# Kernel tuning notes

Measured on AMD Instinct MI355X. Metric: run time of the kernel, lower is better.

Reference implementation:

```python
import jax, jax.numpy as jnp
import numpy as np

B, IN, H, OUT, RANK = 2048, 256, 128, 128, 8
EPS = 1e-5

def setup_inputs() -> dict:
    key = jax.random.key(0)
    ks = jax.random.split(key, 9)
    inv = lambda n: 1.0 / np.sqrt(n)
    return {
        "X": jax.random.normal(ks[0], (B, IN), jnp.float32),
        "W1": jax.random.uniform(ks[1], (IN, H), jnp.float32, -inv(IN), inv(IN)),
        "b1": jnp.zeros((H,), jnp.float32),
        "W2": jax.random.uniform(ks[2], (IN, OUT), jnp.float32, -inv(IN), inv(IN)),
        "b2": jnp.zeros((OUT,), jnp.float32),
        "W3": jax.random.uniform(ks[3], (H, OUT), jnp.float32, -inv(H), inv(H)),
        "b3": jnp.zeros((OUT,), jnp.float32),
        "P": jax.random.normal(ks[4], (RANK, H, H, H), jnp.float32),  # (rank, p, q, k)
        "gz": jnp.ones((H,), jnp.float32),
        "bz": jnp.zeros((H,), jnp.float32),
        "gy": jnp.ones((H,), jnp.float32),
        "by": jnp.zeros((H,), jnp.float32),
    }

def _bn(x, g, b):
    # training-mode BatchNorm1d: batch stats, biased variance
    m = x.mean(axis=0)
    v = x.var(axis=0)
    return (x - m) * jax.lax.rsqrt(v + EPS) * g + b

def reference(X, W1, b1, W2, b2, W3, b3, P, gz, bz, gy, by):
    Z = jax.nn.relu(X @ W1 + b1)               # (B, H); dropout = identity (eval)

    def step(carry, Pi):
        Zi, Y = carry
        # batch_quadratic: out[b,k] = sum_{p,q} Zi[b,p] * Pi[p,q,k] * Z[b,q]
        Zi = jnp.einsum('bp,pqk,bq->bk', Zi, Pi, Z)
        Zi = _bn(Zi, gz, bz)
        return (Zi, Y + Zi / RANK), None

    Y0 = jnp.zeros((X.shape[0], H), X.dtype)
    (_, Y), _ = jax.lax.scan(step, (Z, Y0), P)
    Y = _bn(Y, gy, by)
    out = jax.nn.relu(jax.nn.relu(Y @ W3 + b3) + jax.nn.relu(X @ W2 + b2))
    return out
```

## Files before the change

### kernel.cpp

```cpp
#include <hip/hip_runtime.h>

typedef __bf16 bf16x8 __attribute__((ext_vector_type(8)));
typedef float  floatx4 __attribute__((ext_vector_type(4)));

constexpr int B_    = 2048;
constexpr int NIN   = 256;
constexpr int H_    = 128;
constexpr int RANK_ = 8;
constexpr float EPS_ = 1e-5f;

__global__ __launch_bounds__(256)
void k_head(const float* __restrict__ X,
            const float* __restrict__ W1, const float* __restrict__ b1,
            const float* __restrict__ W2, const float* __restrict__ b2,
            const float* __restrict__ P,
            float* __restrict__ Z, float* __restrict__ R2, __bf16* __restrict__ Zbf,
            __bf16* __restrict__ Pperm, float* __restrict__ stats ) {
    __shared__ float smem[10240];
    const int bx = blockIdx.x, t = threadIdx.x;

    if (bx < RANK_ + 1) stats[bx * 256 + t] = 0.f;

    if ((bx & 3) == 0) {
        const int b0 = (bx >> 2) * 8;
        float* sX  = smem;
        float* sW1 = smem + 2048;
        float* sW2 = smem + 6144;
        for (int e = t; e < 2048; e += 256) {
            const int row = e >> 8, i = e & 255;
            sX[e] = X[(size_t)(b0 + row) * NIN + i];
        }
        const int col = t & 127, rh = t >> 7;
        float s1[4] = {0.f, 0.f, 0.f, 0.f}, s2[4] = {0.f, 0.f, 0.f, 0.f};
        for (int c = 0; c < 8; ++c) {
            __syncthreads();
#pragma unroll
            for (int q = 0; q < 4; ++q) {
                const int idx = q * 256 + t;
                const int i = idx >> 5, c4 = idx & 31;
                *(float4*)&sW1[i * 128 + c4 * 4] =
                    *(const float4*)&W1[(size_t)(c * 32 + i) * H_ + c4 * 4];
                *(float4*)&sW2[i * 128 + c4 * 4] =
                    *(const float4*)&W2[(size_t)(c * 32 + i) * H_ + c4 * 4];
            }
            __syncthreads();
#pragma unroll 4
            for (int i = 0; i < 32; ++i) {
                const float w1 = sW1[i * 128 + col];
                const float w2 = sW2[i * 128 + col];
#pragma unroll
                for (int j = 0; j < 4; ++j) {
                    const float x = sX[(rh * 4 + j) * 256 + c * 32 + i];
                    s1[j] = fmaf(x, w1, s1[j]);
                    s2[j] = fmaf(x, w2, s2[j]);
                }
            }
        }
#pragma unroll
        for (int j = 0; j < 4; ++j) {
            const int b = b0 + rh * 4 + j;
            const float z = fmaxf(s1[j] + b1[col], 0.f);
            const float r = fmaxf(s2[j] + b2[col], 0.f);
            Z[(size_t)b * H_ + col]   = z;
            Zbf[(size_t)b * H_ + col] = (__bf16)z;
            R2[(size_t)b * H_ + col]  = r;
        }
        __syncthreads();
    }
    {
        float* sT = smem;
        const int r = bx >> 7, p = bx & 127;
        const float4* Pp4 = (const float4*)(P + ((size_t)r * H_ + p) * (H_ * H_));
        __bf16* dst = Pperm + (size_t)r * (H_ * H_ * H_);
        const int L = t & 63, quad = L >> 4, lo = L & 15, g0 = t >> 6;
#pragma unroll
        for (int s = 0; s < 4; ++s) {
#pragma unroll
            for (int it = 0; it < 4; ++it) {
                const int idx = it * 256 + t;
                const int q = idx >> 5, k4 = idx & 31;
                const float4 v = Pp4[(size_t)(s * 32 + q) * 32 + k4];
                float* d = sT + q * 129 + k4 * 4;
                d[0] = v.x; d[1] = v.y; d[2] = v.z; d[3] = v.w;
            }
            __syncthreads();
#pragma unroll
            for (int gg = 0; gg < 2; ++gg) {
                const int g = g0 + 4 * gg;
                __bf16 v8[8];
#pragma unroll
                for (int j = 0; j < 8; ++j)
                    v8[j] = (__bf16)sT[(quad * 8 + j) * 129 + g * 16 + lo];
                *(bf16x8*)(dst + (((size_t)(g * 128 + p) * 4 + s) * 64 + L) * 8) =
                    *(const bf16x8*)v8;
            }
            __syncthreads();
        }
    }
}

__global__ __launch_bounds__(1024, 1)
void k_rank(const __bf16* __restrict__ Pr, const __bf16* __restrict__ Zbf,
            const float* __restrict__ prevT, const float* __restrict__ prevStats,
            const float* __restrict__ gz, const float* __restrict__ bz,
            float* __restrict__ T, float* __restrict__ stats,
            float* __restrict__ Y, const int ymode) {
    __shared__ float smem[16672];
    const int kg = blockIdx.x, mblk = blockIdx.y, b0 = mblk * 64;
    const int t = threadIdx.x;
    const int w = t >> 6, L = t & 63, quad = L >> 4, lo = L & 15;

    float* sAl = smem + 16384; float* sBe = smem + 16512;
    if (t < 128) {
        if (ymode == 0) { sAl[t] = 1.f; sBe[t] = 0.f; }
        else {
            const float s1 = prevStats[t], s2 = prevStats[128 + t];
            const float mm = s1 * (1.f / B_);
            const float var = s2 * (1.f / B_) - mm * mm;
            const float a = rsqrtf(var + EPS_) * gz[t];
            sAl[t] = a; sBe[t] = bz[t] - mm * a;
        }
    }
    bf16x8 A[4][4];
#pragma unroll
    for (int mt = 0; mt < 4; ++mt)
#pragma unroll
        for (int ks = 0; ks < 4; ++ks)
            A[mt][ks] = *(const bf16x8*)(Zbf + (size_t)(b0 + mt * 16 + lo) * H_ + ks * 32 + quad * 8);
    __syncthreads();
    {
        const int sp = t & 127, rr = t >> 7;
        const float a = sAl[sp], be = sBe[sp];
#pragma unroll
        for (int i = 0; i < 8; ++i) {
            const int row = rr + 8 * i;
            const float zin = fmaf(prevT[(size_t)(b0 + row) * H_ + sp], a, be);
            smem[sp * 68 + row] = zin;
            if (kg == 0 && ymode != 0) {
                float* yp = Y + (size_t)(b0 + row) * H_ + sp;
                *yp = (ymode == 1) ? zin * (1.f / RANK_) : fmaf(zin, 1.f / RANK_, *yp);
            }
        }
    }
    __syncthreads();

    floatx4 acc[4];
#pragma unroll
    for (int mt = 0; mt < 4; ++mt) acc[mt] = (floatx4){0.f, 0.f, 0.f, 0.f};

    const bf16x8* Pb = (const bf16x8*)Pr;
    const size_t wb = ((size_t)kg * 128 + w * 8) * 4;
    for (int pp = 0; pp < 8; ++pp) {
        bf16x8 Bf[4];
#pragma unroll
        for (int s = 0; s < 4; ++s)
            Bf[s] = Pb[(wb + (size_t)pp * 4 + s) * 64 + L];
        const int p = w * 8 + pp;
#pragma unroll
        for (int mt = 0; mt < 4; ++mt) {
            floatx4 S = (floatx4){0.f, 0.f, 0.f, 0.f};
#pragma unroll
            for (int ks = 0; ks < 4; ++ks)
                S = __builtin_amdgcn_mfma_f32_16x16x32_bf16(A[mt][ks], Bf[ks], S, 0, 0, 0);
            const floatx4 zi = *(const floatx4*)&smem[p * 68 + mt * 16 + quad * 4];
            acc[mt] += zi * S;
        }
    }
    __syncthreads();
#pragma unroll
    for (int mt = 0; mt < 4; ++mt)
#pragma unroll
        for (int i = 0; i < 4; ++i)
            smem[w * 1024 + (mt * 4 + i) * 64 + L] = acc[mt][i];
    if (t < 32) smem[16640 + t] = 0.f;
    __syncthreads();

    float v = 0.f;
#pragma unroll
    for (int q = 0; q < 16; ++q) v += smem[q * 1024 + t];
    const int j = t >> 6, L2 = t & 63;
    const int row = b0 + (j >> 2) * 16 + (L2 >> 4) * 4 + (j & 3);
    const int col = kg * 16 + (L2 & 15);
    T[(size_t)row * H_ + col] = v;
    float cs = v, cs2 = v * v;
    cs  += __shfl_xor(cs, 16);  cs  += __shfl_xor(cs, 32);
    cs2 += __shfl_xor(cs2, 16); cs2 += __shfl_xor(cs2, 32);
    if (L2 < 16) { atomicAdd(&smem[16640 + L2], cs); atomicAdd(&smem[16656 + L2], cs2); }
    __syncthreads();
    if (t < 16)      atomicAdd(&stats[kg * 16 + t],            smem[16640 + t]);
    else if (t < 32) atomicAdd(&stats[128 + kg * 16 + t - 16], smem[16640 + t]);
}

__global__ __launch_bounds__(256)
void k_y(const float* __restrict__ T7, const float* __restrict__ s7,
         const float* __restrict__ gz, const float* __restrict__ bz,
         float* __restrict__ Y, float* __restrict__ ysums) {
    __shared__ float sAl[128], sBe[128], red[256];
    const int bx = blockIdx.x, t = threadIdx.x;
    if (t < 128) {
        const float s1 = s7[t], s2 = s7[128 + t];
        const float mm = s1 * (1.f / B_);
        const float var = s2 * (1.f / B_) - mm * mm;
        const float a = rsqrtf(var + EPS_) * gz[t];
        sAl[t] = a; sBe[t] = bz[t] - mm * a;
    }
    red[t] = 0.f;
    __syncthreads();
    const int col = t & 127, half = t >> 7;
    const float a = sAl[col], be = sBe[col];
    float ps = 0.f, ps2 = 0.f;
    for (int i = 0; i < 16; ++i) {
        const int b = bx * 32 + half + 2 * i;
        const size_t gi = (size_t)b * H_ + col;
        const float y = Y[gi] + fmaf(T7[gi], a, be) * (1.f / RANK_);
        Y[gi] = y;
        ps += y; ps2 += y * y;
    }
    atomicAdd(&red[col],       half == 0 ? ps  : 0.f);
    atomicAdd(&red[128 + col], half == 0 ? ps2 : 0.f);
    __syncthreads();
    atomicAdd(&red[col],       half == 1 ? ps  : 0.f);
    atomicAdd(&red[128 + col], half == 1 ? ps2 : 0.f);
    __syncthreads();
    if (t < 128) {
        atomicAdd(&ysums[t],       red[t]);
        atomicAdd(&ysums[128 + t], red[128 + t]);
    }
}

__global__ __launch_bounds__(256)
void k_out(const float* __restrict__ Y, const float* __restrict__ ystats,
           const float* __restrict__ gy, const float* __restrict__ by,
           const float* __restrict__ W3, const float* __restrict__ b3,
           const float* __restrict__ R2, float* __restrict__ out) {
    __shared__ float sy[8 * 132];
    const int bx = blockIdx.x, t = threadIdx.x;
    const int col = t & 127, rh = t >> 7;
    const int b0 = bx * 8;
    const float mm = ystats[col] * (1.f / B_);
    const float var = ystats[128 + col] * (1.f / B_) - mm * mm;
    const float ay = rsqrtf(var + EPS_) * gy[col];
    const float bb = by[col] - mm * ay;
#pragma unroll
    for (int i = 0; i < 4; ++i) {
        const int row = rh + 2 * i;
        sy[row * 132 + col] = fmaf(Y[(size_t)(b0 + row) * H_ + col], ay, bb);
    }
    __syncthreads();
#pragma unroll
    for (int j = 0; j < 4; ++j) {
        const int row = rh * 4 + j;
        float s = 0.f;
        const float* syr = sy + row * 132;
#pragma unroll 8
        for (int h = 0; h < H_; ++h)
            s = fmaf(syr[h], W3[h * H_ + col], s);
        const size_t gi = (size_t)(b0 + row) * H_ + col;
        out[gi] = fmaxf(fmaxf(s + b3[col], 0.f) + R2[gi], 0.f);
    }
}

extern "C" void kernel_launch(void* const* d_in, const int* in_sizes, int n_in,
                              void* d_out, int out_size, void* d_ws, size_t ws_size,
                              hipStream_t stream) {
    const float* X  = (const float*)d_in[0];
    const float* W1 = (const float*)d_in[1];
    const float* b1 = (const float*)d_in[2];
    const float* W2 = (const float*)d_in[3];
    const float* b2 = (const float*)d_in[4];
    const float* W3 = (const float*)d_in[5];
    const float* b3 = (const float*)d_in[6];
    const float* P  = (const float*)d_in[7];
    const float* gz = (const float*)d_in[8];
    const float* bz = (const float*)d_in[9];
    const float* gy = (const float*)d_in[10];
    const float* by = (const float*)d_in[11];
    float* out = (float*)d_out;

    const size_t rankElems = (size_t)H_ * H_ * H_;

    char* wsb = (char*)d_ws;
    float* Z      = (float*)wsb;   wsb += (size_t)B_ * H_ * 4;
    float* R2     = (float*)wsb;   wsb += (size_t)B_ * H_ * 4;
    float* Y      = (float*)wsb;   wsb += (size_t)B_ * H_ * 4;
    float* stats  = (float*)wsb;   wsb += (size_t)(RANK_ + 1) * 256 * 4;
    float* T      = (float*)wsb;   wsb += (size_t)RANK_ * B_ * H_ * 4;
    __bf16* Zbf   = (__bf16*)wsb;  wsb += (size_t)B_ * H_ * 2;
    __bf16* Pperm = (__bf16*)wsb;

    float* ysums = stats + RANK_ * 256;

    k_head<<<1024, 256, 0, stream>>>(X, W1, b1, W2, b2, P, Z, R2, Zbf, Pperm, stats);

    for (int r = 0; r < RANK_; ++r) {
        const float* prevT = (r == 0) ? Z : (T + (size_t)(r - 1) * B_ * H_);
        const float* prevS = (r == 0) ? stats : (stats + (r - 1) * 256);
        const int ymode = (r == 0) ? 0 : (r == 1 ? 1 : 2);
        k_rank<<<dim3(8, 32), 1024, 0, stream>>>(Pperm + (size_t)r * rankElems, Zbf,
                                                 prevT, prevS, gz, bz,
                                                 T + (size_t)r * B_ * H_, stats + r * 256,
                                                 Y, ymode);
    }

    k_y<<<64, 256, 0, stream>>>(T + (size_t)7 * B_ * H_, stats + 7 * 256, gz, bz, Y, ysums);
    k_out<<<256, 256, 0, stream>>>(Y, ysums, gy, by, W3, b3, R2, out);
}
```

Measured before the change: 324.2 us.

## Convert next rank's P slice inside k_rank to overlap with compute

The head kernel now converts only rank 0 of P to permuted bf16, and handles 4 batch rows per block across all 512 blocks with weights read directly from global memory. Each k_rank launch converts the next rank's P slice after finishing its own work, so the large P conversion is spread across the rank loop instead of sitting in the head kernel. This adds extra global traffic and barriers to every k_rank launch. It relies on launch ordering on the stream so that rank r+1 data is ready before it is used.

```diff
diff --git a/kernel.cpp b/kernel.cpp
--- a/kernel.cpp
+++ b/kernel.cpp
@@ -16,85 +16,61 @@
             const float* __restrict__ P,
             float* __restrict__ Z, float* __restrict__ R2, __bf16* __restrict__ Zbf,
             __bf16* __restrict__ Pperm, float* __restrict__ stats ) {
-    __shared__ float smem[10240];
+    __shared__ float smem[4160];
     const int bx = blockIdx.x, t = threadIdx.x;
 
     if (bx < RANK_ + 1) stats[bx * 256 + t] = 0.f;
 
-    if ((bx & 3) == 0) {
-        const int b0 = (bx >> 2) * 8;
-        float* sX  = smem;
-        float* sW1 = smem + 2048;
-        float* sW2 = smem + 6144;
-        for (int e = t; e < 2048; e += 256) {
-            const int row = e >> 8, i = e & 255;
-            sX[e] = X[(size_t)(b0 + row) * NIN + i];
-        }
+    {
+        const int b0 = bx * 4;
+#pragma unroll
+        for (int i = 0; i < 4; ++i) {
+            const int e = i * 256 + t;
+            smem[e] = X[(size_t)(b0 + (e >> 8)) * NIN + (e & 255)];
+        }
+        __syncthreads();
         const int col = t & 127, rh = t >> 7;
-        float s1[4] = {0.f, 0.f, 0.f, 0.f}, s2[4] = {0.f, 0.f, 0.f, 0.f};
-        for (int c = 0; c < 8; ++c) {
-            __syncthreads();
-#pragma unroll
-            for (int q = 0; q < 4; ++q) {
-                const int idx = q * 256 + t;
-                const int i = idx >> 5, c4 = idx & 31;
-                *(float4*)&sW1[i * 128 + c4 * 4] =
-                    *(const float4*)&W1[(size_t)(c * 32 + i) * H_ + c4 * 4];
-                *(float4*)&sW2[i * 128 + c4 * 4] =
-                    *(const float4*)&W2[(size_t)(c * 32 + i) * H_ + c4 * 4];
-            }
-            __syncthreads();
-#pragma unroll 4
-            for (int i = 0; i < 32; ++i) {
-                const float w1 = sW1[i * 128 + col];
-                const float w2 = sW2[i * 128 + col];
-#pragma unroll
-                for (int j = 0; j < 4; ++j) {
-                    const float x = sX[(rh * 4 + j) * 256 + c * 32 + i];
-                    s1[j] = fmaf(x, w1, s1[j]);
-                    s2[j] = fmaf(x, w2, s2[j]);
-                }
-            }
-        }
-#pragma unroll
-        for (int j = 0; j < 4; ++j) {
-            const int b = b0 + rh * 4 + j;
-            const float z = fmaxf(s1[j] + b1[col], 0.f);
-            const float r = fmaxf(s2[j] + b2[col], 0.f);
-            Z[(size_t)b * H_ + col]   = z;
-            Zbf[(size_t)b * H_ + col] = (__bf16)z;
-            R2[(size_t)b * H_ + col]  = r;
-        }
+        float s1a = 0.f, s2a = 0.f, s1b = 0.f, s2b = 0.f;
+        const float* sxa = smem + rh * 256;
+        const float* sxb = smem + (rh + 2) * 256;
+#pragma unroll 8
+        for (int i = 0; i < NIN; ++i) {
+            const float w1 = W1[i * H_ + col];
+            const float w2 = W2[i * H_ + col];
+            s1a = fmaf(sxa[i], w1, s1a);  s2a = fmaf(sxa[i], w2, s2a);
+            s1b = fmaf(sxb[i], w1, s1b);  s2b = fmaf(sxb[i], w2, s2b);
+        }
+        const int ba = b0 + rh, bb = b0 + rh + 2;
+        const float za = fmaxf(s1a + b1[col], 0.f), ra = fmaxf(s2a + b2[col], 0.f);
+        const float zb = fmaxf(s1b + b1[col], 0.f), rb = fmaxf(s2b + b2[col], 0.f);
+        Z[(size_t)ba * H_ + col] = za;  Zbf[(size_t)ba * H_ + col] = (__bf16)za;
+        R2[(size_t)ba * H_ + col] = ra;
+        Z[(size_t)bb * H_ + col] = zb;  Zbf[(size_t)bb * H_ + col] = (__bf16)zb;
+        R2[(size_t)bb * H_ + col] = rb;
         __syncthreads();
     }
     {
-        float* sT = smem;
-        const int r = bx >> 7, p = bx & 127;
-        const float4* Pp4 = (const float4*)(P + ((size_t)r * H_ + p) * (H_ * H_));
-        __bf16* dst = Pperm + (size_t)r * (H_ * H_ * H_);
+        const int p = bx >> 2, s = bx & 3;
+        const float4* Pp4 = (const float4*)(P + (size_t)p * (H_ * H_));
         const int L = t & 63, quad = L >> 4, lo = L & 15, g0 = t >> 6;
 #pragma unroll
-        for (int s = 0; s < 4; ++s) {
-#pragma unroll
-            for (int it = 0; it < 4; ++it) {
-                const int idx = it * 256 + t;
-                const int q = idx >> 5, k4 = idx & 31;
-                const float4 v = Pp4[(size_t)(s * 32 + q) * 32 + k4];
-                float* d = sT + q * 129 + k4 * 4;
-                d[0] = v.x; d[1] = v.y; d[2] = v.z; d[3] = v.w;
-            }
-            __syncthreads();
-#pragma unroll
-            for (int gg = 0; gg < 2; ++gg) {
-                const int g = g0 + 4 * gg;
-                __bf16 v8[8];
-#pragma unroll
-                for (int j = 0; j < 8; ++j)
-                    v8[j] = (__bf16)sT[(quad * 8 + j) * 129 + g * 16 + lo];
-                *(bf16x8*)(dst + (((size_t)(g * 128 + p) * 4 + s) * 64 + L) * 8) =
-                    *(const bf16x8*)v8;
-            }
-            __syncthreads();
+        for (int it = 0; it < 4; ++it) {
+            const int idx = it * 256 + t;
+            const int q = idx >> 5, k4 = idx & 31;
+            const float4 v = Pp4[(size_t)(s * 32 + q) * 32 + k4];
+            float* d = smem + q * 129 + k4 * 4;
+            d[0] = v.x; d[1] = v.y; d[2] = v.z; d[3] = v.w;
+        }
+        __syncthreads();
+#pragma unroll
+        for (int gg = 0; gg < 2; ++gg) {
+            const int g = g0 + 4 * gg;
+            __bf16 v8[8];
+#pragma unroll
+            for (int j = 0; j < 8; ++j)
+                v8[j] = (__bf16)smem[(quad * 8 + j) * 129 + g * 16 + lo];
+            *(bf16x8*)(Pperm + (((size_t)(g * 128 + p) * 4 + s) * 64 + L) * 8) =
+                *(const bf16x8*)v8;
         }
     }
 }
@@ -104,7 +80,9 @@
             const float* __restrict__ prevT, const float* __restrict__ prevStats,
             const float* __restrict__ gz, const float* __restrict__ bz,
             float* __restrict__ T, float* __restrict__ stats,
-            float* __restrict__ Y, const int ymode) {
+            float* __restrict__ Y, const int ymode,
+            const float* __restrict__ Pnext, __bf16* __restrict__ PpermNext,
+            const int doPconv) {
     __shared__ float smem[16672];
     const int kg = blockIdx.x, mblk = blockIdx.y, b0 = mblk * 64;
     const int t = threadIdx.x;
@@ -189,6 +167,30 @@
     __syncthreads();
     if (t < 16)      atomicAdd(&stats[kg * 16 + t],            smem[16640 + t]);
     else if (t < 32) atomicAdd(&stats[128 + kg * 16 + t - 16], smem[16640 + t]);
+
+    if (doPconv) {
+        const int lid = kg * 32 + mblk;
+        const int p = lid >> 1;
+        const int s0 = (lid & 1) << 1;
+        const float4* Pp4 = (const float4*)(Pnext + (size_t)p * (H_ * H_));
+        const int q = t >> 5, k4 = t & 31;
+        for (int ss = 0; ss < 2; ++ss) {
+            const int s = s0 + ss;
+            const float4 vv = Pp4[(size_t)(s * 32 + q) * 32 + k4];
+            __syncthreads();
+            float* d = smem + q * 129 + k4 * 4;
+            d[0] = vv.x; d[1] = vv.y; d[2] = vv.z; d[3] = vv.w;
+            __syncthreads();
+            if (w < 8) {
+                __bf16 v8[8];
+#pragma unroll
+                for (int jj = 0; jj < 8; ++jj)
+                    v8[jj] = (__bf16)smem[(quad * 8 + jj) * 129 + w * 16 + lo];
+                *(bf16x8*)(PpermNext + (((size_t)(w * 128 + p) * 4 + s) * 64 + L) * 8) =
+                    *(const bf16x8*)v8;
+            }
+        }
+    }
 }
 
 __global__ __launch_bounds__(256)
@@ -290,16 +292,20 @@
 
     float* ysums = stats + RANK_ * 256;
 
-    k_head<<<1024, 256, 0, stream>>>(X, W1, b1, W2, b2, P, Z, R2, Zbf, Pperm, stats);
+    k_head<<<512, 256, 0, stream>>>(X, W1, b1, W2, b2, P, Z, R2, Zbf, Pperm, stats);
 
     for (int r = 0; r < RANK_; ++r) {
         const float* prevT = (r == 0) ? Z : (T + (size_t)(r - 1) * B_ * H_);
         const float* prevS = (r == 0) ? stats : (stats + (r - 1) * 256);
         const int ymode = (r == 0) ? 0 : (r == 1 ? 1 : 2);
+        const int doP = (r < RANK_ - 1) ? 1 : 0;
         k_rank<<<dim3(8, 32), 1024, 0, stream>>>(Pperm + (size_t)r * rankElems, Zbf,
                                                  prevT, prevS, gz, bz,
                                                  T + (size_t)r * B_ * H_, stats + r * 256,
-                                                 Y, ymode);
+                                                 Y, ymode,
+                                                 P + (size_t)(r + 1) * rankElems,
+                                                 Pperm + (size_t)(r + 1) * rankElems,
+                                                 doP);
     }
 
     k_y<<<64, 256, 0, stream>>>(T + (size_t)7 * B_ * H_, stats + 7 * 256, gz, bz, Y, ysums);
```

After: 317.8 us. -2.0%, faster.
